# Kernel tuning notes

Measured on AMD Instinct MI355X. Metric: run time of the kernel, lower is better.

The kernel has to match this reference:

```python
import jax, jax.numpy as jnp
import numpy as np

NUM_HEADS = 4   # forced by reshape(B, N, num_heads, C) of a dim*4 projection
BN_EPS = 1e-5


def _chamfer(a, b):
    # a, b: [B, N, 3] -> symmetric chamfer distance (mean of nearest sq-dists)
    d = (jnp.sum(a ** 2, -1)[:, :, None] + jnp.sum(b ** 2, -1)[:, None, :]
         - 2.0 * jnp.einsum('bnc,bmc->bnm', a, b))
    return jnp.mean(jnp.min(d, axis=2)) + jnp.mean(jnp.min(d, axis=1))


def _forward(xs, pc1, bn_gamma, bn_beta, q_w, kv_w, proj_w, proj_b, map_w, map_b):
    B, F, C, N = xs.shape
    H = NUM_HEADS
    scale = C ** -0.5  # head_dim == dim in this module (full-dim heads)

    def per_item(x):  # x: [F, C, N]
        # BatchNorm1d in eval mode (running_mean=0, running_var=1)
        xn = (x / jnp.sqrt(1.0 + BN_EPS)) * bn_gamma[:, None] + bn_beta[:, None]
        xn = xn.transpose(0, 2, 1)                 # [F, N, C]
        xr = xn[::-1]                              # flip over frame axis
        q = (xn @ q_w.T).reshape(F, N, H, C).transpose(0, 2, 1, 3)        # [F,H,N,C]
        kv = (xr @ kv_w.T).reshape(F, N, 2, H, C).transpose(2, 0, 3, 1, 4)
        k, v = kv[0], kv[1]                        # [F,H,N,C]
        attn = jax.nn.softmax(jnp.einsum('fhnc,fhmc->fhnm', q, k) * scale, axis=-1)
        o = jnp.einsum('fhnm,fhmc->fhnc', attn, v).transpose(0, 2, 1, 3)  # [F,N,H,C]
        xa = (o[0] + o[1]).transpose(1, 0, 2)      # [H, N, C]: sum of first two frames
        xa = xa @ proj_w.T + proj_b                # [H, N, C] x_appearance
        fr = xa @ map_w.T + map_b                  # [H, N, 3] frames (mapping_xyz)
        return xa, fr

    xa, frames = jax.vmap(per_item)(xs)            # [B,H,N,C], [B,H,N,3]
    pc1t = pc1.transpose(0, 2, 1)                  # [B, N, 3]
    loss = _chamfer(pc1t + frames[:, 0], pc1t)
    return xa[:, 1:], frames[:, 1:], loss


def setup_inputs() -> dict:
    key = jax.random.key(0)
    ks = jax.random.split(key, 8)
    B, F, C, N = 2, 4, 64, 2048
    return {
        'xs': jax.random.normal(ks[0], (B, F, C, N), jnp.float32),
        'pc1': jax.random.normal(ks[1], (B, 3, N), jnp.float32),
        'pc2': jax.random.normal(ks[2], (B, 3, N), jnp.float32),
        'bn_gamma': jnp.ones((C,), jnp.float32),
        'bn_beta': jnp.zeros((C,), jnp.float32),
        'q_w': 0.02 * jax.random.normal(ks[3], (4 * C, C), jnp.float32),
        'kv_w': 0.02 * jax.random.normal(ks[4], (8 * C, C), jnp.float32),
        'proj_w': 0.02 * jax.random.normal(ks[5], (C, C), jnp.float32),
        'proj_b': jnp.zeros((C,), jnp.float32),
        'map_w': 0.02 * jax.random.normal(ks[6], (3, C), jnp.float32),
        'map_b': jnp.zeros((3,), jnp.float32),
    }


def reference(xs, pc1, pc2, bn_gamma, bn_beta, q_w, kv_w, proj_w, proj_b, map_w, map_b):
    # pc2 is accepted by the torch forward but unused in its body
    return _forward(xs, pc1, bn_gamma, bn_beta, q_w, kv_w, proj_w, proj_b, map_w, map_b)
```

## Files before the change

### kernel.cpp

```cpp
#include <hip/hip_runtime.h>
#include <hip/hip_bf16.h>

#define NPTS 2048
#define LOG2E 1.4426950408889634f
#define NJC 16
#define JCH 128
#define KSPLIT 8

typedef short bf16x8 __attribute__((ext_vector_type(8)));
typedef float f32x4 __attribute__((ext_vector_type(4)));
typedef unsigned uint32x4 __attribute__((ext_vector_type(4)));
typedef __attribute__((address_space(3))) char lds_char;
typedef __attribute__((address_space(1))) const char glob_char;

union PBU { uint32x4 u; bf16x8 v; };

static __device__ __forceinline__ unsigned cvt_pk_bf16(float a, float b) {
    unsigned r;
    asm("v_cvt_pk_bf16_f32 %0, %1, %2" : "=v"(r) : "v"(a), "v"(b));
    return r;
}
static __device__ __forceinline__ float b2f(unsigned short u) {
    return __uint_as_float((unsigned)u << 16);
}

__global__ void prep_weights(const float* __restrict__ gamma, const float* __restrict__ beta,
                             const float* __restrict__ q_w, const float* __restrict__ kv_w,
                             float* __restrict__ Wp, float* __restrict__ bp) {
    int j = blockIdx.x * blockDim.x + threadIdx.x;
    if (j >= 768) return;
    const float inv = 1.0f / sqrtf(1.0f + 1e-5f);
    const float* src;
    float scale;
    if (j < 256) { src = q_w + j * 64;          scale = 0.125f * LOG2E; }
    else         { src = kv_w + (j - 256) * 64; scale = 1.0f; }
    float b = 0.f;
    for (int c = 0; c < 64; ++c) {
        float w = src[c];
        Wp[j * 64 + c] = w * gamma[c] * inv * scale;
        b += w * beta[c];
    }
    bp[j] = b * scale;
}

__global__ __launch_bounds__(256) void qkv_gemm(const float* __restrict__ xs,
                                                const float* __restrict__ Wp,
                                                const float* __restrict__ bp,
                                                __hip_bfloat16* __restrict__ Qg,
                                                __hip_bfloat16* __restrict__ Kg,
                                                __hip_bfloat16* __restrict__ Vtg) {
    const int bf = blockIdx.z;
    const int b = bf >> 1, f01 = bf & 1;
    const int jt = blockIdx.y;
    const int f_src = (jt < 4) ? f01 : (3 - f01);
    const int n0 = blockIdx.x * 64;
    const float* __restrict__ A = xs + (size_t)((b * 4 + f_src) * 64) * NPTS;

    __shared__ float As[64][68];
    __shared__ float Ws[64][68];

    const int t = threadIdx.x;
    const int tx = t & 15, ty = t >> 4;

    for (int r = 0; r < 4; ++r) {
        int row = ty + 16 * r;
        int col = tx * 4;
        *(float4*)&As[row][col] = *(const float4*)&A[(size_t)row * NPTS + n0 + col];
        *(float4*)&Ws[row][col] = *(const float4*)&Wp[(size_t)(jt * 64 + row) * 64 + col];
    }
    __syncthreads();

    float acc[4][4];
#pragma unroll
    for (int jj = 0; jj < 4; ++jj) {
        float bv = bp[jt * 64 + tx + 16 * jj];
#pragma unroll
        for (int i = 0; i < 4; ++i) acc[i][jj] = bv;
    }
    for (int c = 0; c < 64; ++c) {
        float a[4], w[4];
#pragma unroll
        for (int i = 0; i < 4; ++i) a[i] = As[c][ty + 16 * i];
#pragma unroll
        for (int jj = 0; jj < 4; ++jj) w[jj] = Ws[tx + 16 * jj][c];
#pragma unroll
        for (int i = 0; i < 4; ++i)
#pragma unroll
            for (int jj = 0; jj < 4; ++jj) acc[i][jj] += a[i] * w[jj];
    }

    if (jt < 8) {
        __hip_bfloat16* __restrict__ dst = (jt < 4 ? Qg : Kg) + (size_t)bf * NPTS * 256;
        const int jb = (jt & 3) * 64;
#pragma unroll
        for (int i = 0; i < 4; ++i) {
            int n = n0 + ty + 16 * i;
#pragma unroll
            for (int jj = 0; jj < 4; ++jj)
                dst[(size_t)n * 256 + jb + tx + 16 * jj] = __float2bfloat16(acc[i][jj]);
        }
    } else {
        __syncthreads();
#pragma unroll
        for (int i = 0; i < 4; ++i)
#pragma unroll
            for (int jj = 0; jj < 4; ++jj)
                As[tx + 16 * jj][ty + 16 * i] = acc[i][jj];
        __syncthreads();
        const int row = t >> 2, c0 = (t & 3) * 16;
        __hip_bfloat16* __restrict__ dst =
            Vtg + ((size_t)bf * 256 + (jt - 8) * 64 + row) * NPTS + n0 + c0;
#pragma unroll
        for (int c = 0; c < 16; ++c) dst[c] = __float2bfloat16(As[row][c0 + c]);
    }
}

__global__ __launch_bounds__(256, 4) void attn_mfma(const __hip_bfloat16* __restrict__ Qg,
                                                    const __hip_bfloat16* __restrict__ Kg,
                                                    const __hip_bfloat16* __restrict__ Vtg,
                                                    __hip_bfloat16* __restrict__ OTb,
                                                    float* __restrict__ Lp) {
    const int combo = blockIdx.x;
    const int bf = combo >> 2, h = combo & 3;
    const int n0 = blockIdx.y * 128;
    const int split = blockIdx.z;
    const int kbase = split * (NPTS / KSPLIT);
    const int NT = NPTS / KSPLIT / 32;

    __shared__ __align__(16) char smem[32768];

    const int t = threadIdx.x;
    const int lane = t & 63, w = t >> 6;
    const int l15 = lane & 15, g = (lane >> 4) & 3;

    const int krow = w * 8 + (lane >> 3), kslot = lane & 7;
    const int vrow = w * 16 + (lane >> 2), vslot = lane & 3;
    const int kcs = (kslot ^ (krow & 7)) * 8;
    const int vcs = (vslot ^ ((vrow >> 1) & 3)) * 8;

    const __hip_bfloat16* qbase =
        Qg + ((size_t)bf * NPTS + n0 + w * 32 + l15) * 256 + h * 64 + g * 8;
    bf16x8 qf[2][2];
    qf[0][0] = *(const bf16x8*)(qbase);
    qf[0][1] = *(const bf16x8*)(qbase + 32);
    qf[1][0] = *(const bf16x8*)(qbase + 16 * 256);
    qf[1][1] = *(const bf16x8*)(qbase + 16 * 256 + 32);

    const __hip_bfloat16* kgb = Kg + (size_t)bf * NPTS * 256 + h * 64;
    const __hip_bfloat16* vgb = Vtg + ((size_t)bf * 256 + h * 64) * NPTS;

    int koff[2][2], voff[4];
#pragma unroll
    for (int tt = 0; tt < 2; ++tt) {
        const int row = tt * 16 + l15;
#pragma unroll
        for (int s = 0; s < 2; ++s)
            koff[tt][s] = row * 128 + (((s * 4 + g) ^ (row & 7)) << 4);
    }
#pragma unroll
    for (int ct = 0; ct < 4; ++ct) {
        const int row = ct * 16 + l15;
        voff[ct] = 4096 + row * 64 + ((g ^ ((row >> 1) & 3)) << 4);
    }

    f32x4 oacc[2][4];
    float lsum[2] = {0.f, 0.f};
#pragma unroll
    for (int f = 0; f < 2; ++f)
#pragma unroll
        for (int r = 0; r < 4; ++r) oacc[f][r] = (f32x4){0.f, 0.f, 0.f, 0.f};

    auto stage = [&](int kt) {
        const int bsel = kt & 3;
        const __hip_bfloat16* ksrc = kgb + (size_t)(kbase + kt * 32 + krow) * 256 + kcs;
        __builtin_amdgcn_global_load_lds((const glob_char*)ksrc,
            (lds_char*)(smem + bsel * 8192 + w * 1024), 16, 0, 0);
        const __hip_bfloat16* vsrc = vgb + (size_t)vrow * NPTS + kbase + kt * 32 + vcs;
        __builtin_amdgcn_global_load_lds((const glob_char*)vsrc,
            (lds_char*)(smem + bsel * 8192 + 4096 + w * 1024), 16, 0, 0);
    };

    auto tile = [&](int kt) {
        const char* B = smem + (kt & 3) * 8192;
        bf16x8 kf[2][2];
#pragma unroll
        for (int tt = 0; tt < 2; ++tt)
#pragma unroll
            for (int s = 0; s < 2; ++s)
                kf[tt][s] = *(const bf16x8*)(B + koff[tt][s]);

        bf16x8 pb[2];
#pragma unroll
        for (int f = 0; f < 2; ++f) {
            f32x4 st0 = (f32x4){0.f, 0.f, 0.f, 0.f}, st1 = st0;
            st0 = __builtin_amdgcn_mfma_f32_16x16x32_bf16(kf[0][0], qf[f][0], st0, 0, 0, 0);
            st0 = __builtin_amdgcn_mfma_f32_16x16x32_bf16(kf[0][1], qf[f][1], st0, 0, 0, 0);
            st1 = __builtin_amdgcn_mfma_f32_16x16x32_bf16(kf[1][0], qf[f][0], st1, 0, 0, 0);
            st1 = __builtin_amdgcn_mfma_f32_16x16x32_bf16(kf[1][1], qf[f][1], st1, 0, 0, 0);
            float p00 = exp2f(st0[0]);
            float p01 = exp2f(st0[1]);
            float p02 = exp2f(st0[2]);
            float p03 = exp2f(st0[3]);
            float p10 = exp2f(st1[0]);
            float p11 = exp2f(st1[1]);
            float p12 = exp2f(st1[2]);
            float p13 = exp2f(st1[3]);
            lsum[f] += ((p00 + p01) + (p02 + p03)) + ((p10 + p11) + (p12 + p13));
            unsigned x0 = cvt_pk_bf16(p00, p01);
            unsigned x1 = cvt_pk_bf16(p02, p03);
            unsigned y0 = cvt_pk_bf16(p10, p11);
            unsigned y1 = cvt_pk_bf16(p12, p13);
            asm("v_permlane32_swap_b32 %0, %1" : "+v"(x0), "+v"(y0));
            asm("v_permlane16_swap_b32 %0, %1" : "+v"(x0), "+v"(y0));
            asm("v_permlane32_swap_b32 %0, %1" : "+v"(x1), "+v"(y1));
            asm("v_permlane16_swap_b32 %0, %1" : "+v"(x1), "+v"(y1));
            PBU pu;
            pu.u = (uint32x4){x0, x1, y0, y1};
            pb[f] = pu.v;
        }

#pragma unroll
        for (int ct = 0; ct < 4; ++ct) {
            bf16x8 vf = *(const bf16x8*)(B + voff[ct]);
            oacc[0][ct] = __builtin_amdgcn_mfma_f32_16x16x32_bf16(vf, pb[0], oacc[0][ct], 0, 0, 0);
            oacc[1][ct] = __builtin_amdgcn_mfma_f32_16x16x32_bf16(vf, pb[1], oacc[1][ct], 0, 0, 0);
        }
    };

    stage(0);
    stage(1);
    for (int kt = 0; kt < NT - 2; ++kt) {
        stage(kt + 2);
        asm volatile("s_waitcnt vmcnt(4)" ::: "memory");
        asm volatile("s_waitcnt lgkmcnt(0)" ::: "memory");
        __builtin_amdgcn_s_barrier();
        asm volatile("" ::: "memory");
        tile(kt);
    }
    asm volatile("s_waitcnt vmcnt(2)" ::: "memory");
    asm volatile("s_waitcnt lgkmcnt(0)" ::: "memory");
    __builtin_amdgcn_s_barrier();
    asm volatile("" ::: "memory");
    tile(NT - 2);
    asm volatile("s_waitcnt vmcnt(0)" ::: "memory");
    asm volatile("s_waitcnt lgkmcnt(0)" ::: "memory");
    __builtin_amdgcn_s_barrier();
    asm volatile("" ::: "memory");
    tile(NT - 1);

    float l0 = lsum[0], l1 = lsum[1];
    l0 += __shfl_xor(l0, 16);
    l0 += __shfl_xor(l0, 32);
    l1 += __shfl_xor(l1, 16);
    l1 += __shfl_xor(l1, 32);
    const int qq = n0 + w * 32 + l15;
    if (g == 0 && lane < 16) {
        Lp[(size_t)(split * 16 + combo) * NPTS + qq] = l0;
        Lp[(size_t)(split * 16 + combo) * NPTS + qq + 16] = l1;
    }

    __hip_bfloat16* __restrict__ Op = OTb + (size_t)(split * 16 + combo) * 64 * NPTS;
#pragma unroll
    for (int ct = 0; ct < 4; ++ct)
#pragma unroll
        for (int r = 0; r < 4; ++r) {
            Op[(size_t)(ct * 16 + g * 4 + r) * NPTS + qq] = __float2bfloat16(oacc[0][ct][r]);
            Op[(size_t)(ct * 16 + g * 4 + r) * NPTS + qq + 16] = __float2bfloat16(oacc[1][ct][r]);
        }
}

__global__ __launch_bounds__(256) void proj_frames(const __hip_bfloat16* __restrict__ OTb,
                                                   const float* __restrict__ Lp,
                                                   const float* __restrict__ proj_w,
                                                   const float* __restrict__ proj_b,
                                                   const float* __restrict__ map_w,
                                                   const float* __restrict__ map_b,
                                                   float* __restrict__ out,
                                                   float* __restrict__ frames0) {
    const int bh = blockIdx.y, b = bh >> 2, h = bh & 3;
    const int n0 = blockIdx.x * 64;
    const int cf0 = (b * 2 + 0) * 4 + h;
    const int cf1 = (b * 2 + 1) * 4 + h;

    __shared__ float Xs[64][68];
    __shared__ float Ws[64][68];
    __shared__ float xaS[64][68];

    const int t = threadIdx.x;
    const int tx = t & 15, ty = t >> 4;
    const int nc = n0 + tx * 4;

    float4 L0 = make_float4(0.f, 0.f, 0.f, 0.f), L1 = L0;
#pragma unroll
    for (int s = 0; s < KSPLIT; ++s) {
        float4 a = *(const float4*)&Lp[(size_t)(s * 16 + cf0) * NPTS + nc];
        L0.x += a.x; L0.y += a.y; L0.z += a.z; L0.w += a.w;
        float4 c = *(const float4*)&Lp[(size_t)(s * 16 + cf1) * NPTS + nc];
        L1.x += c.x; L1.y += c.y; L1.z += c.z; L1.w += c.w;
    }
    float4 inv0 = make_float4(1.f / L0.x, 1.f / L0.y, 1.f / L0.z, 1.f / L0.w);
    float4 inv1 = make_float4(1.f / L1.x, 1.f / L1.y, 1.f / L1.z, 1.f / L1.w);

    for (int r = 0; r < 4; ++r) {
        int row = ty + 16 * r, col = tx * 4;
        float x0 = 0.f, x1 = 0.f, x2 = 0.f, x3 = 0.f;
        float y0 = 0.f, y1 = 0.f, y2 = 0.f, y3 = 0.f;
#pragma unroll
        for (int s = 0; s < KSPLIT; ++s) {
            ushort4 u0 = *(const ushort4*)&OTb[((size_t)(s * 16 + cf0) * 64 + row) * NPTS + n0 + col];
            ushort4 u1 = *(const ushort4*)&OTb[((size_t)(s * 16 + cf1) * 64 + row) * NPTS + n0 + col];
            x0 += b2f(u0.x); x1 += b2f(u0.y); x2 += b2f(u0.z); x3 += b2f(u0.w);
            y0 += b2f(u1.x); y1 += b2f(u1.y); y2 += b2f(u1.z); y3 += b2f(u1.w);
        }
        Xs[row][col + 0] = x0 * inv0.x + y0 * inv1.x;
        Xs[row][col + 1] = x1 * inv0.y + y1 * inv1.y;
        Xs[row][col + 2] = x2 * inv0.z + y2 * inv1.z;
        Xs[row][col + 3] = x3 * inv0.w + y3 * inv1.w;
        *(float4*)&Ws[row][col] = *(const float4*)&proj_w[(size_t)row * 64 + col];
    }
    __syncthreads();

    float acc[4][4];
#pragma unroll
    for (int jj = 0; jj < 4; ++jj) {
        float bv = proj_b[tx + 16 * jj];
#pragma unroll
        for (int i = 0; i < 4; ++i) acc[i][jj] = bv;
    }
    for (int c = 0; c < 64; ++c) {
        float a[4], w[4];
#pragma unroll
        for (int i = 0; i < 4; ++i) a[i] = Xs[c][ty + 16 * i];
#pragma unroll
        for (int jj = 0; jj < 4; ++jj) w[jj] = Ws[tx + 16 * jj][c];
#pragma unroll
        for (int i = 0; i < 4; ++i)
#pragma unroll
            for (int jj = 0; jj < 4; ++jj) acc[i][jj] += a[i] * w[jj];
    }

#pragma unroll
    for (int i = 0; i < 4; ++i)
#pragma unroll
        for (int jj = 0; jj < 4; ++jj)
            xaS[ty + 16 * i][tx + 16 * jj] = acc[i][jj];

    if (h >= 1) {
        float* __restrict__ xa_out = out + (size_t)(b * 3 + h - 1) * NPTS * 64;
#pragma unroll
        for (int i = 0; i < 4; ++i)
#pragma unroll
            for (int jj = 0; jj < 4; ++jj)
                xa_out[(size_t)(n0 + ty + 16 * i) * 64 + tx + 16 * jj] = acc[i][jj];
    }
    __syncthreads();

    if (t < 192) {
        int r = t / 3, j = t % 3;
        float s = map_b[j];
        for (int c = 0; c < 64; ++c) s += xaS[r][c] * map_w[j * 64 + c];
        int n = n0 + r;
        if (h == 0) frames0[((size_t)b * NPTS + n) * 3 + j] = s;
        else        out[786432 + ((size_t)(b * 3 + h - 1) * NPTS + n) * 3 + j] = s;
    }
}

__global__ __launch_bounds__(256) void chamfer_partial(const float* __restrict__ pc1,
                                                       const float* __restrict__ frames0,
                                                       float* __restrict__ partial) {
    const int z = blockIdx.z;
    const int dir = z >> 1, b = z & 1;
    const int i = blockIdx.x * 256 + threadIdx.x;
    const int j0 = blockIdx.y * JCH;
    const float* __restrict__ px = pc1 + (size_t)b * 3 * NPTS;
    const float* __restrict__ fr = frames0 + (size_t)b * NPTS * 3;

    __shared__ float4 sj[JCH];
    if (threadIdx.x < JCH) {
        int jj = j0 + threadIdx.x;
        float bx = px[jj], by = px[NPTS + jj], bz = px[2 * NPTS + jj];
        if (dir == 1) { bx += fr[jj * 3]; by += fr[jj * 3 + 1]; bz += fr[jj * 3 + 2]; }
        sj[threadIdx.x] = make_float4(bx, by, bz, bx * bx + by * by + bz * bz);
    }
    float ax = px[i], ay = px[NPTS + i], az = px[2 * NPTS + i];
    if (dir == 0) { ax += fr[i * 3]; ay += fr[i * 3 + 1]; az += fr[i * 3 + 2]; }
    const float a2 = ax * ax + ay * ay + az * az;
    __syncthreads();

    float best = 1e30f;
#pragma unroll 4
    for (int k = 0; k < JCH; ++k) {
        float4 p = sj[k];
        float d = a2 + p.w - 2.0f * (ax * p.x + ay * p.y + az * p.z);
        best = fminf(best, d);
    }
    partial[((size_t)z * NJC + blockIdx.y) * NPTS + i] = best;
}

__global__ __launch_bounds__(256) void chamfer_minsum(const float* __restrict__ partial,
                                                      double* __restrict__ sums) {
    const int gid = blockIdx.x * 256 + threadIdx.x;
    const int z = gid >> 11, i = gid & 2047;
    float best = 1e30f;
#pragma unroll
    for (int c = 0; c < NJC; ++c)
        best = fminf(best, partial[((size_t)z * NJC + c) * NPTS + i]);
    __shared__ double sm[256];
    sm[threadIdx.x] = (double)best;
    __syncthreads();
    for (int off = 128; off > 0; off >>= 1) {
        if (threadIdx.x < off) sm[threadIdx.x] += sm[threadIdx.x + off];
        __syncthreads();
    }
    if (threadIdx.x == 0) sums[blockIdx.x] = sm[0];
}

__global__ void chamfer_final(const double* __restrict__ sums, float* __restrict__ loss_out) {
    if (threadIdx.x == 0) {
        double s = 0.0;
        for (int k = 0; k < 32; ++k) s += sums[k];
        loss_out[0] = (float)(s / 4096.0);
    }
}

extern "C" void kernel_launch(void* const* d_in, const int* in_sizes, int n_in,
                              void* d_out, int out_size, void* d_ws, size_t ws_size,
                              hipStream_t stream) {
    const float* xs     = (const float*)d_in[0];
    const float* pc1    = (const float*)d_in[1];
    const float* gamma  = (const float*)d_in[3];
    const float* beta   = (const float*)d_in[4];
    const float* q_w    = (const float*)d_in[5];
    const float* kv_w   = (const float*)d_in[6];
    const float* proj_w = (const float*)d_in[7];
    const float* proj_b = (const float*)d_in[8];
    const float* map_w  = (const float*)d_in[9];
    const float* map_b  = (const float*)d_in[10];
    float* out = (float*)d_out;

    char* ws = (char*)d_ws;
    __hip_bfloat16* Qg  = (__hip_bfloat16*)(ws);
    __hip_bfloat16* Kg  = (__hip_bfloat16*)(ws + 4194304);
    __hip_bfloat16* Vtg = (__hip_bfloat16*)(ws + 8388608);
    __hip_bfloat16* OTb = (__hip_bfloat16*)(ws + 12582912);
    float* Wp      = (float*)(ws + 46137344);
    float* bp      = (float*)(ws + 46333952);
    float* frames0 = (float*)(ws + 46337024);
    float* partial = (float*)(ws + 46386176);
    double* sums   = (double*)(ws + 46910464);
    float* Lp      = (float*)(ws + 46910720);

    hipLaunchKernelGGL(prep_weights, dim3(3), dim3(256), 0, stream,
                       gamma, beta, q_w, kv_w, Wp, bp);
    hipLaunchKernelGGL(qkv_gemm, dim3(32, 12, 4), dim3(256), 0, stream,
                       xs, Wp, bp, Qg, Kg, Vtg);
    hipLaunchKernelGGL(attn_mfma, dim3(16, 16, KSPLIT), dim3(256), 0, stream,
                       Qg, Kg, Vtg, OTb, Lp);
    hipLaunchKernelGGL(proj_frames, dim3(32, 8), dim3(256), 0, stream,
                       OTb, Lp, proj_w, proj_b, map_w, map_b, out, frames0);
    hipLaunchKernelGGL(chamfer_partial, dim3(NPTS / 256, NJC, 4), dim3(256), 0, stream,
                       pc1, frames0, partial);
    hipLaunchKernelGGL(chamfer_minsum, dim3(32), dim3(256), 0, stream,
                       partial, sums);
    hipLaunchKernelGGL(chamfer_final, dim3(1), dim3(64), 0, stream,
                       sums, out + 823296);
}
```

Baseline: 85.59 us.

## Move QKV projection to bf16 MFMA with pre-normalized transposed input

Adds a kernel that applies the BatchNorm scale and shift to xs, then writes it transposed as bf16 [frame][n][c]. The fp32 LDS-tiled QKV GEMM is replaced by bf16 MFMA 16x16x32 operating directly on the transposed input and on bf16 weights, which removes LDS staging and scalar FMA work. It costs one extra kernel launch and an extra round trip through memory for xT, and rounding the input and weights to bf16 lowers precision. The Lp write guard is also loosened so every lane under 16 writes, not only lanes with g == 0.

```diff
diff --git a/kernel.cpp b/kernel.cpp
--- a/kernel.cpp
+++ b/kernel.cpp
@@ -24,28 +24,61 @@
     return __uint_as_float((unsigned)u << 16);
 }
 
-__global__ void prep_weights(const float* __restrict__ gamma, const float* __restrict__ beta,
-                             const float* __restrict__ q_w, const float* __restrict__ kv_w,
-                             float* __restrict__ Wp, float* __restrict__ bp) {
+__global__ void prep_weights(const float* __restrict__ q_w, const float* __restrict__ kv_w,
+                             __hip_bfloat16* __restrict__ Wpb) {
     int j = blockIdx.x * blockDim.x + threadIdx.x;
     if (j >= 768) return;
-    const float inv = 1.0f / sqrtf(1.0f + 1e-5f);
     const float* src;
     float scale;
     if (j < 256) { src = q_w + j * 64;          scale = 0.125f * LOG2E; }
     else         { src = kv_w + (j - 256) * 64; scale = 1.0f; }
-    float b = 0.f;
-    for (int c = 0; c < 64; ++c) {
-        float w = src[c];
-        Wp[j * 64 + c] = w * gamma[c] * inv * scale;
-        b += w * beta[c];
-    }
-    bp[j] = b * scale;
-}
-
-__global__ __launch_bounds__(256) void qkv_gemm(const float* __restrict__ xs,
-                                                const float* __restrict__ Wp,
-                                                const float* __restrict__ bp,
+    for (int c = 0; c < 64; ++c)
+        Wpb[j * 64 + c] = __float2bfloat16(src[c] * scale);
+}
+
+__global__ __launch_bounds__(256) void xt_kernel(const float* __restrict__ xs,
+                                                 const float* __restrict__ gamma,
+                                                 const float* __restrict__ beta,
+                                                 __hip_bfloat16* __restrict__ xT) {
+    const int fr = blockIdx.y;
+    const int n0 = blockIdx.x * 64;
+    const float* __restrict__ A = xs + (size_t)fr * 64 * NPTS;
+
+    __shared__ float As[64][68];
+    __shared__ float sg[64], sb[64];
+
+    const int t = threadIdx.x;
+    if (t < 64) {
+        const float inv = 1.0f / sqrtf(1.0f + 1e-5f);
+        sg[t] = gamma[t] * inv;
+        sb[t] = beta[t];
+    }
+    const int tx = t & 15, ty = t >> 4;
+    for (int r = 0; r < 4; ++r) {
+        int row = ty + 16 * r, col = tx * 4;
+        *(float4*)&As[row][col] = *(const float4*)&A[(size_t)row * NPTS + n0 + col];
+    }
+    __syncthreads();
+
+    const int nl = t >> 2, c0 = (t & 3) * 16;
+    bf16x8 v0, v1;
+#pragma unroll
+    for (int j = 0; j < 8; ++j) {
+        float a = As[c0 + j][nl] * sg[c0 + j] + sb[c0 + j];
+        v0[j] = (short)__bfloat16_as_ushort(__float2bfloat16(a));
+    }
+#pragma unroll
+    for (int j = 0; j < 8; ++j) {
+        float a = As[c0 + 8 + j][nl] * sg[c0 + 8 + j] + sb[c0 + 8 + j];
+        v1[j] = (short)__bfloat16_as_ushort(__float2bfloat16(a));
+    }
+    __hip_bfloat16* dst = xT + ((size_t)fr * NPTS + n0 + nl) * 64 + c0;
+    *(bf16x8*)(dst) = v0;
+    *(bf16x8*)(dst + 8) = v1;
+}
+
+__global__ __launch_bounds__(256) void qkv_mfma(const __hip_bfloat16* __restrict__ xT,
+                                                const __hip_bfloat16* __restrict__ Wpb,
                                                 __hip_bfloat16* __restrict__ Qg,
                                                 __hip_bfloat16* __restrict__ Kg,
                                                 __hip_bfloat16* __restrict__ Vtg) {
@@ -54,64 +87,50 @@
     const int jt = blockIdx.y;
     const int f_src = (jt < 4) ? f01 : (3 - f01);
     const int n0 = blockIdx.x * 64;
-    const float* __restrict__ A = xs + (size_t)((b * 4 + f_src) * 64) * NPTS;
-
-    __shared__ float As[64][68];
-    __shared__ float Ws[64][68];
-
-    const int t = threadIdx.x;
-    const int tx = t & 15, ty = t >> 4;
-
-    for (int r = 0; r < 4; ++r) {
-        int row = ty + 16 * r;
-        int col = tx * 4;
-        *(float4*)&As[row][col] = *(const float4*)&A[(size_t)row * NPTS + n0 + col];
-        *(float4*)&Ws[row][col] = *(const float4*)&Wp[(size_t)(jt * 64 + row) * 64 + col];
-    }
-    __syncthreads();
-
-    float acc[4][4];
-#pragma unroll
-    for (int jj = 0; jj < 4; ++jj) {
-        float bv = bp[jt * 64 + tx + 16 * jj];
-#pragma unroll
-        for (int i = 0; i < 4; ++i) acc[i][jj] = bv;
-    }
-    for (int c = 0; c < 64; ++c) {
-        float a[4], w[4];
-#pragma unroll
-        for (int i = 0; i < 4; ++i) a[i] = As[c][ty + 16 * i];
-#pragma unroll
-        for (int jj = 0; jj < 4; ++jj) w[jj] = Ws[tx + 16 * jj][c];
-#pragma unroll
-        for (int i = 0; i < 4; ++i)
-#pragma unroll
-            for (int jj = 0; jj < 4; ++jj) acc[i][jj] += a[i] * w[jj];
-    }
+
+    const int t = threadIdx.x, lane = t & 63, w = t >> 6;
+    const int l15 = lane & 15, g = (lane >> 4) & 3;
+
+    const __hip_bfloat16* __restrict__ xfb = xT + (size_t)(b * 4 + f_src) * NPTS * 64;
 
     if (jt < 8) {
+        const __hip_bfloat16* wp = Wpb + (size_t)(jt * 64 + w * 16 + l15) * 64 + g * 8;
+        bf16x8 wf0 = *(const bf16x8*)(wp);
+        bf16x8 wf1 = *(const bf16x8*)(wp + 32);
         __hip_bfloat16* __restrict__ dst = (jt < 4 ? Qg : Kg) + (size_t)bf * NPTS * 256;
-        const int jb = (jt & 3) * 64;
-#pragma unroll
-        for (int i = 0; i < 4; ++i) {
-            int n = n0 + ty + 16 * i;
-#pragma unroll
-            for (int jj = 0; jj < 4; ++jj)
-                dst[(size_t)n * 256 + jb + tx + 16 * jj] = __float2bfloat16(acc[i][jj]);
+        const int jb = (jt & 3) * 64 + w * 16 + g * 4;
+#pragma unroll
+        for (int nt = 0; nt < 4; ++nt) {
+            const __hip_bfloat16* xp = xfb + (size_t)(n0 + nt * 16 + l15) * 64 + g * 8;
+            bf16x8 xf0 = *(const bf16x8*)(xp);
+            bf16x8 xf1 = *(const bf16x8*)(xp + 32);
+            f32x4 d = (f32x4){0.f, 0.f, 0.f, 0.f};
+            d = __builtin_amdgcn_mfma_f32_16x16x32_bf16(wf0, xf0, d, 0, 0, 0);
+            d = __builtin_amdgcn_mfma_f32_16x16x32_bf16(wf1, xf1, d, 0, 0, 0);
+            uint2 pv;
+            pv.x = cvt_pk_bf16(d[0], d[1]);
+            pv.y = cvt_pk_bf16(d[2], d[3]);
+            *(uint2*)&dst[(size_t)(n0 + nt * 16 + l15) * 256 + jb] = pv;
         }
     } else {
-        __syncthreads();
-#pragma unroll
-        for (int i = 0; i < 4; ++i)
-#pragma unroll
-            for (int jj = 0; jj < 4; ++jj)
-                As[tx + 16 * jj][ty + 16 * i] = acc[i][jj];
-        __syncthreads();
-        const int row = t >> 2, c0 = (t & 3) * 16;
-        __hip_bfloat16* __restrict__ dst =
-            Vtg + ((size_t)bf * 256 + (jt - 8) * 64 + row) * NPTS + n0 + c0;
-#pragma unroll
-        for (int c = 0; c < 16; ++c) dst[c] = __float2bfloat16(As[row][c0 + c]);
+        const __hip_bfloat16* xp = xfb + (size_t)(n0 + w * 16 + l15) * 64 + g * 8;
+        bf16x8 xf0 = *(const bf16x8*)(xp);
+        bf16x8 xf1 = *(const bf16x8*)(xp + 32);
+        __hip_bfloat16* __restrict__ dst = Vtg + (size_t)bf * 256 * NPTS;
+#pragma unroll
+        for (int tj = 0; tj < 4; ++tj) {
+            const int ch = (jt - 8) * 64 + tj * 16 + l15;
+            const __hip_bfloat16* wp = Wpb + (size_t)(512 + ch) * 64 + g * 8;
+            bf16x8 wf0 = *(const bf16x8*)(wp);
+            bf16x8 wf1 = *(const bf16x8*)(wp + 32);
+            f32x4 d = (f32x4){0.f, 0.f, 0.f, 0.f};
+            d = __builtin_amdgcn_mfma_f32_16x16x32_bf16(xf0, wf0, d, 0, 0, 0);
+            d = __builtin_amdgcn_mfma_f32_16x16x32_bf16(xf1, wf1, d, 0, 0, 0);
+            uint2 pv;
+            pv.x = cvt_pk_bf16(d[0], d[1]);
+            pv.y = cvt_pk_bf16(d[2], d[3]);
+            *(uint2*)&dst[(size_t)ch * NPTS + n0 + w * 16 + g * 4] = pv;
+        }
     }
 }
 
@@ -254,7 +273,7 @@
     l1 += __shfl_xor(l1, 16);
     l1 += __shfl_xor(l1, 32);
     const int qq = n0 + w * 32 + l15;
-    if (g == 0 && lane < 16) {
+    if (lane < 16) {
         Lp[(size_t)(split * 16 + combo) * NPTS + qq] = l0;
         Lp[(size_t)(split * 16 + combo) * NPTS + qq + 16] = l1;
     }
@@ -443,17 +462,19 @@
     __hip_bfloat16* Kg  = (__hip_bfloat16*)(ws + 4194304);
     __hip_bfloat16* Vtg = (__hip_bfloat16*)(ws + 8388608);
     __hip_bfloat16* OTb = (__hip_bfloat16*)(ws + 12582912);
-    float* Wp      = (float*)(ws + 46137344);
-    float* bp      = (float*)(ws + 46333952);
-    float* frames0 = (float*)(ws + 46337024);
-    float* partial = (float*)(ws + 46386176);
-    double* sums   = (double*)(ws + 46910464);
-    float* Lp      = (float*)(ws + 46910720);
+    __hip_bfloat16* Wpb = (__hip_bfloat16*)(ws + 46137344);
+    __hip_bfloat16* xT  = (__hip_bfloat16*)(ws + 46235648);
+    float* frames0 = (float*)(ws + 48332800);
+    float* partial = (float*)(ws + 48381952);
+    double* sums   = (double*)(ws + 48906240);
+    float* Lp      = (float*)(ws + 48906496);
 
     hipLaunchKernelGGL(prep_weights, dim3(3), dim3(256), 0, stream,
-                       gamma, beta, q_w, kv_w, Wp, bp);
-    hipLaunchKernelGGL(qkv_gemm, dim3(32, 12, 4), dim3(256), 0, stream,
-                       xs, Wp, bp, Qg, Kg, Vtg);
+                       q_w, kv_w, Wpb);
+    hipLaunchKernelGGL(xt_kernel, dim3(32, 8), dim3(256), 0, stream,
+                       xs, gamma, beta, xT);
+    hipLaunchKernelGGL(qkv_mfma, dim3(32, 12, 4), dim3(256), 0, stream,
+                       xT, Wpb, Qg, Kg, Vtg);
     hipLaunchKernelGGL(attn_mfma, dim3(16, 16, KSPLIT), dim3(256), 0, stream,
                        Qg, Kg, Vtg, OTb, Lp);
     hipLaunchKernelGGL(proj_frames, dim3(32, 8), dim3(256), 0, stream,
```

Result: faster. 80.43 us (-6.0%).
